# Kernel tuning notes

Measured on AMD Instinct MI355X. Metric: run time of the kernel, lower is better.

## Reference

```python
import jax, jax.numpy as jnp
import numpy as np

N = 50000      # nodes
E = 800000     # edges (before self loops)
F_IN = 128
HID = 32
HEADS = 4
C = 64         # num_classes
SLOPE = 0.2    # LeakyReLU negative slope (PyG GATConv default)


def setup_inputs() -> dict:
    key = jax.random.key(0)
    ks = jax.random.split(key, 16)
    def nrm(k, shape, scale=0.1):
        return jax.random.normal(k, shape, jnp.float32) * scale
    x = jax.random.normal(ks[0], (N, F_IN), jnp.float32)
    edge_index = jax.random.randint(ks[1], (2, E), 0, N, jnp.int32)
    # layer 1: F_IN -> HID per head, concat -> HEADS*HID
    w1 = nrm(ks[2], (F_IN, HEADS * HID)); as1 = nrm(ks[3], (HEADS, HID)); ad1 = nrm(ks[4], (HEADS, HID)); b1 = nrm(ks[5], (HEADS * HID,))
    # layer 2: HEADS*HID -> HID per head, concat
    w2 = nrm(ks[6], (HEADS * HID, HEADS * HID)); as2 = nrm(ks[7], (HEADS, HID)); ad2 = nrm(ks[8], (HEADS, HID)); b2 = nrm(ks[9], (HEADS * HID,))
    # layer 3: HEADS*HID -> C, single head, no concat (mean)
    w3 = nrm(ks[10], (HEADS * HID, C)); as3 = nrm(ks[11], (1, C)); ad3 = nrm(ks[12], (1, C)); b3 = nrm(ks[13], (C,))
    return {"x": x, "edge_index": edge_index,
            "w1": w1, "as1": as1, "ad1": ad1, "b1": b1,
            "w2": w2, "as2": as2, "ad2": ad2, "b2": b2,
            "w3": w3, "as3": as3, "ad3": ad3, "b3": b3}


def gat_conv(x, src, dst, W, a_src, a_dst, bias, heads, oc, concat):
    n = x.shape[0]
    h = (x @ W).reshape(n, heads, oc)                       # [N,H,F]
    al_s = jnp.einsum('nhf,hf->nh', h, a_src)               # [N,H]
    al_d = jnp.einsum('nhf,hf->nh', h, a_dst)
    e = jax.nn.leaky_relu(al_s[src] + al_d[dst], SLOPE)     # [E,H]
    # segment softmax over incoming edges per destination node
    m = jax.ops.segment_max(e, dst, num_segments=n)
    e = jnp.exp(e - m[dst])
    denom = jax.ops.segment_sum(e, dst, num_segments=n)
    alpha = e / denom[dst]                                  # [E,H]
    out = jax.ops.segment_sum(h[src] * alpha[:, :, None], dst, num_segments=n)  # [N,H,F]
    out = out.reshape(n, heads * oc) if concat else out.mean(axis=1)
    return out + bias


def reference(x, edge_index, w1, as1, ad1, b1, w2, as2, ad2, b2, w3, as3, ad3, b3):
    n = x.shape[0]
    loops = jnp.arange(n, dtype=edge_index.dtype)
    src = jnp.concatenate([edge_index[0], loops])           # add self loops (PyG default)
    dst = jnp.concatenate([edge_index[1], loops])
    h = gat_conv(x, src, dst, w1, as1, ad1, b1, HEADS, HID, True)
    h = jax.nn.relu(h)                                      # dropout is identity in eval
    h = gat_conv(h, src, dst, w2, as2, ad2, b2, HEADS, HID, True)
    h = jax.nn.relu(h)
    h = gat_conv(h, src, dst, w3, as3, ad3, b3, 1, C, False)
    return jax.nn.log_softmax(h, axis=1)
```

## Files before the change

### kernel.cpp

```cpp
#include <hip/hip_runtime.h>
#include <hip/hip_bf16.h>
#include <math.h>

#define SLOPE 0.2f
typedef unsigned int uint_t;
typedef unsigned short ushort_t;

static __device__ __forceinline__ float lrelu(float v) { return v > 0.f ? v : SLOPE * v; }
static __device__ __forceinline__ ushort_t f2b(float f) {
  uint_t u = __float_as_uint(f);
  u += 0x7fffu + ((u >> 16) & 1u);
  return (ushort_t)(u >> 16);
}


__global__ __launch_bounds__(256) void hist_kernel(const int* __restrict__ ei,
                                                   int* __restrict__ ts,
                                                   int E, int N, int NB, int NBUCK) {
  __shared__ int h[256];
  int tid = threadIdx.x, b = blockIdx.x;
  h[tid] = 0;
  __syncthreads();
  int ET = E + N;
  int base = b * 4096;
#pragma unroll
  for (int j = 0; j < 16; ++j) {
    int i = base + j * 256 + tid;
    if (i < ET) {
      int d = (i < E) ? ei[E + i] : (i - E);
      atomicAdd(&h[d >> 8], 1);
    }
  }
  __syncthreads();
  if (tid < NBUCK) ts[tid * NB + b] = h[tid];
}

__global__ __launch_bounds__(256) void scan1(int* __restrict__ a, int* __restrict__ bsum, int L) {
  int tid = threadIdx.x;
  int base = blockIdx.x * 1024 + tid * 4;
  int c0 = (base + 0 < L) ? a[base + 0] : 0;
  int c1 = (base + 1 < L) ? a[base + 1] : 0;
  int c2 = (base + 2 < L) ? a[base + 2] : 0;
  int c3 = (base + 3 < L) ? a[base + 3] : 0;
  int s = c0 + c1 + c2 + c3;
  int lane = tid & 63, wid = tid >> 6;
  int pre = s;
#pragma unroll
  for (int off = 1; off < 64; off <<= 1) {
    int t = __shfl_up(pre, off);
    if (lane >= off) pre += t;
  }
  __shared__ int wsum[4];
  if (lane == 63) wsum[wid] = pre;
  __syncthreads();
  int woff = 0;
#pragma unroll
  for (int w = 0; w < 4; ++w) woff += (w < wid) ? wsum[w] : 0;
  int excl = woff + pre - s;
  if (base + 0 < L) a[base + 0] = excl;
  if (base + 1 < L) a[base + 1] = excl + c0;
  if (base + 2 < L) a[base + 2] = excl + c0 + c1;
  if (base + 3 < L) a[base + 3] = excl + c0 + c1 + c2;
  if (tid == 255) bsum[blockIdx.x] = wsum[0] + wsum[1] + wsum[2] + wsum[3];
}

__global__ __launch_bounds__(1024) void scan2(int* __restrict__ bsum, int nb) {
  __shared__ int sh[1024];
  int tid = threadIdx.x;
  int v = (tid < nb) ? bsum[tid] : 0;
  sh[tid] = v;
  __syncthreads();
  for (int off = 1; off < 1024; off <<= 1) {
    int add = (tid >= off) ? sh[tid - off] : 0;
    __syncthreads();
    sh[tid] += add;
    __syncthreads();
  }
  if (tid < nb) bsum[tid] = sh[tid] - v;
}

__global__ __launch_bounds__(256) void scan3(int* __restrict__ a, const int* __restrict__ bsum, int L) {
  int tid = threadIdx.x;
  int base = blockIdx.x * 1024 + tid * 4;
  if (base >= L) return;
  int off = bsum[blockIdx.x];
#pragma unroll
  for (int j = 0; j < 4; ++j)
    if (base + j < L) a[base + j] += off;
}

__global__ __launch_bounds__(256) void part_kernel(const int* __restrict__ ei,
                                                   const int* __restrict__ ts,
                                                   uint_t* __restrict__ tmp,
                                                   int E, int N, int NB, int NBUCK) {
  __shared__ int bin[256];
  int tid = threadIdx.x, b = blockIdx.x;
  if (tid < NBUCK) bin[tid] = ts[tid * NB + b];
  __syncthreads();
  int ET = E + N;
  int base = b * 4096;
#pragma unroll
  for (int j = 0; j < 16; ++j) {
    int i = base + j * 256 + tid;
    if (i < ET) {
      int s, d;
      if (i < E) { s = ei[i]; d = ei[E + i]; } else { s = i - E; d = i - E; }
      int pos = atomicAdd(&bin[d >> 8], 1);
      tmp[pos] = ((uint_t)d << 16) | (uint_t)s;
    }
  }
}

__global__ __launch_bounds__(256) void bucket_kernel(const uint_t* __restrict__ tmp,
                                                     const int* __restrict__ ts,
                                                     int* __restrict__ rowptr,
                                                     int* __restrict__ esrc,
                                                     int N, int NB, int NBUCK, int ET) {
  __shared__ int h[256], pref[256], rank[256];
  __shared__ int wsum[4];
  int tid = threadIdx.x, d = blockIdx.x;
  int start = ts[d * NB];
  int end = (d == NBUCK - 1) ? ET : ts[(d + 1) * NB];
  h[tid] = 0; rank[tid] = 0;
  __syncthreads();
  for (int i = start + tid; i < end; i += 256)
    atomicAdd(&h[(tmp[i] >> 16) & 255], 1);
  __syncthreads();
  int v = h[tid];
  int lane = tid & 63, wid = tid >> 6;
  int inc = v;
#pragma unroll
  for (int off = 1; off < 64; off <<= 1) {
    int t = __shfl_up(inc, off);
    if (lane >= off) inc += t;
  }
  if (lane == 63) wsum[wid] = inc;
  __syncthreads();
  int woff = 0;
#pragma unroll
  for (int w = 0; w < 4; ++w) woff += (w < wid) ? wsum[w] : 0;
  pref[tid] = woff + inc - v;
  __syncthreads();
  int idx = d * 256 + tid;
  if (idx <= N) rowptr[idx] = start + pref[tid];
  for (int i = start + tid; i < end; i += 256) {
    uint_t v2 = tmp[i];
    int low = (v2 >> 16) & 255;
    int r = atomicAdd(&rank[low], 1);
    esrc[start + pref[low] + r] = (int)(v2 & 0xffffu);
  }
}


template<int OC, bool BF16IN>
__global__ __launch_bounds__(256) void gemm_tile(const void* __restrict__ Xv,
                                                 const float* __restrict__ W,
                                                 ushort_t* __restrict__ H, int N) {
  const int K = 128;
  const int CT = OC / 4;
  const int RPT = 64 / (256 / CT);
  __shared__ float xs[K][68];
  int tid = threadIdx.x;
  long row0 = (long)blockIdx.x * 64;
  if (BF16IN) {
    const ushort_t* X = (const ushort_t*)Xv;
#pragma unroll
    for (int i = 0; i < 4; ++i) {
      int flat = i * 256 + tid;
      int r = flat & 63, kc = flat >> 6;
      long row = row0 + r;
      long rr = row < N ? row : (long)(N - 1);
      uint4 v = *(const uint4*)(X + rr * K + kc * 8);
      uint_t vv[4] = {v.x, v.y, v.z, v.w};
#pragma unroll
      for (int j = 0; j < 4; ++j) {
        xs[kc * 8 + j * 2 + 0][r] = __uint_as_float(vv[j] << 16);
        xs[kc * 8 + j * 2 + 1][r] = __uint_as_float(vv[j] & 0xffff0000u);
      }
    }
  } else {
    const float* X = (const float*)Xv;
#pragma unroll
    for (int i = 0; i < 8; ++i) {
      int flat = i * 256 + tid;
      int r = flat & 63, kc = flat >> 6;
      long row = row0 + r;
      long rr = row < N ? row : (long)(N - 1);
      float4 xv = *(const float4*)(X + rr * K + kc * 4);
      xs[kc * 4 + 0][r] = xv.x;
      xs[kc * 4 + 1][r] = xv.y;
      xs[kc * 4 + 2][r] = xv.z;
      xs[kc * 4 + 3][r] = xv.w;
    }
  }
  __syncthreads();
  int ct = tid % CT;
  int rg = tid / CT;
  int c0 = ct * 4;
  int r0 = rg * RPT;
  float acc[RPT][4];
#pragma unroll
  for (int i = 0; i < RPT; ++i)
    for (int j = 0; j < 4; ++j) acc[i][j] = 0.f;
#pragma unroll 4
  for (int k = 0; k < K; ++k) {
    float4 wv = *(const float4*)(W + (long)k * OC + c0);
    const float4* xr = (const float4*)(&xs[k][r0]);
#pragma unroll
    for (int i4 = 0; i4 < RPT / 4; ++i4) {
      float4 xv = xr[i4];
      float xa[4] = {xv.x, xv.y, xv.z, xv.w};
#pragma unroll
      for (int j = 0; j < 4; ++j) {
        int i = i4 * 4 + j;
        acc[i][0] = fmaf(xa[j], wv.x, acc[i][0]);
        acc[i][1] = fmaf(xa[j], wv.y, acc[i][1]);
        acc[i][2] = fmaf(xa[j], wv.z, acc[i][2]);
        acc[i][3] = fmaf(xa[j], wv.w, acc[i][3]);
      }
    }
  }
#pragma unroll
  for (int i = 0; i < RPT; ++i) {
    long row = row0 + r0 + i;
    if (row < N) {
      ushort4 o = {f2b(acc[i][0]), f2b(acc[i][1]), f2b(acc[i][2]), f2b(acc[i][3])};
      *(ushort4*)(H + row * OC + c0) = o;
    }
  }
}


__global__ void al_kernel4(const ushort_t* __restrict__ h, const float* __restrict__ a_s,
                           const float* __restrict__ a_d, float* __restrict__ als,
                           float* __restrict__ ald, int N) {
  int tid = threadIdx.x;
  int n = blockIdx.x * 16 + (tid >> 4);
  int sl = tid & 15, hd = sl >> 2;
  if (n >= N) return;
  uint4 v = *(const uint4*)(h + (long)n * 128 + sl * 8);
  uint_t vv[4] = {v.x, v.y, v.z, v.w};
  const float* sp = a_s + hd * 32 + (sl & 3) * 8;
  const float* dp = a_d + hd * 32 + (sl & 3) * 8;
  float vs = 0.f, vd = 0.f;
#pragma unroll
  for (int j = 0; j < 4; ++j) {
    float h0 = __uint_as_float(vv[j] << 16);
    float h1 = __uint_as_float(vv[j] & 0xffff0000u);
    vs = fmaf(h0, sp[j * 2 + 0], vs); vs = fmaf(h1, sp[j * 2 + 1], vs);
    vd = fmaf(h0, dp[j * 2 + 0], vd); vd = fmaf(h1, dp[j * 2 + 1], vd);
  }
#pragma unroll
  for (int off = 1; off <= 2; off <<= 1) {
    vs += __shfl_xor(vs, off);
    vd += __shfl_xor(vd, off);
  }
  if ((sl & 3) == 0) { als[(long)n * 4 + hd] = vs; ald[(long)n * 4 + hd] = vd; }
}

__global__ void al_kernel1(const ushort_t* __restrict__ h, const float* __restrict__ a_s,
                           const float* __restrict__ a_d, float* __restrict__ als,
                           float* __restrict__ ald, int N) {
  int tid = threadIdx.x;
  int n = blockIdx.x * 32 + (tid >> 3);
  int sl = tid & 7;
  if (n >= N) return;
  uint4 v = *(const uint4*)(h + (long)n * 64 + sl * 8);
  uint_t vv[4] = {v.x, v.y, v.z, v.w};
  const float* sp = a_s + sl * 8;
  const float* dp = a_d + sl * 8;
  float vs = 0.f, vd = 0.f;
#pragma unroll
  for (int j = 0; j < 4; ++j) {
    float h0 = __uint_as_float(vv[j] << 16);
    float h1 = __uint_as_float(vv[j] & 0xffff0000u);
    vs = fmaf(h0, sp[j * 2 + 0], vs); vs = fmaf(h1, sp[j * 2 + 1], vs);
    vd = fmaf(h0, dp[j * 2 + 0], vd); vd = fmaf(h1, dp[j * 2 + 1], vd);
  }
#pragma unroll
  for (int off = 1; off <= 4; off <<= 1) {
    vs += __shfl_xor(vs, off);
    vd += __shfl_xor(vd, off);
  }
  if (sl == 0) { als[n] = vs; ald[n] = vd; }
}


__global__ __launch_bounds__(256) void gat_agg128(const ushort_t* __restrict__ h,
    const float* __restrict__ als, const float* __restrict__ ald,
    const int* __restrict__ rowptr, const int* __restrict__ esrc,
    const float* __restrict__ bias, ushort_t* __restrict__ out, int N) {
  int tid = threadIdx.x;
  int n = blockIdx.x * 8 + (tid >> 5);
  int l = tid & 31;
  int slot = l >> 4, sl = l & 15, hd = sl >> 2;
  if (n >= N) return;
  int beg = rowptr[n], end = rowptr[n + 1];
  float aldv = ald[(long)n * 4 + hd];
  float den = 0.f;
  float acc[8] = {0.f, 0.f, 0.f, 0.f, 0.f, 0.f, 0.f, 0.f};
  for (int e = beg + slot; e < end; e += 2) {
    int s = esrc[e];
    float p = __expf(lrelu(als[(long)s * 4 + hd] + aldv));
    den += p;
    uint4 v = *(const uint4*)(h + (long)s * 128 + sl * 8);
    uint_t vv[4] = {v.x, v.y, v.z, v.w};
#pragma unroll
    for (int j = 0; j < 4; ++j) {
      acc[2 * j + 0] = fmaf(p, __uint_as_float(vv[j] << 16), acc[2 * j + 0]);
      acc[2 * j + 1] = fmaf(p, __uint_as_float(vv[j] & 0xffff0000u), acc[2 * j + 1]);
    }
  }
  den += __shfl_xor(den, 16);
#pragma unroll
  for (int j = 0; j < 8; ++j) acc[j] += __shfl_xor(acc[j], 16);
  if (slot == 0) {
    float inv = 1.f / den;
    float4 bv0 = *(const float4*)(bias + sl * 8);
    float4 bv1 = *(const float4*)(bias + sl * 8 + 4);
    float bb[8] = {bv0.x, bv0.y, bv0.z, bv0.w, bv1.x, bv1.y, bv1.z, bv1.w};
    uint_t pk[4];
#pragma unroll
    for (int j = 0; j < 4; ++j) {
      float v0 = fmaxf(fmaf(acc[2 * j + 0], inv, bb[2 * j + 0]), 0.f);
      float v1 = fmaxf(fmaf(acc[2 * j + 1], inv, bb[2 * j + 1]), 0.f);
      pk[j] = (uint_t)f2b(v0) | ((uint_t)f2b(v1) << 16);
    }
    uint4 pv = {pk[0], pk[1], pk[2], pk[3]};
    *(uint4*)(out + (long)n * 128 + sl * 8) = pv;
  }
}

__global__ __launch_bounds__(256) void gat_agg64_lsm(const ushort_t* __restrict__ h,
    const float* __restrict__ als, const float* __restrict__ ald,
    const int* __restrict__ rowptr, const int* __restrict__ esrc,
    const float* __restrict__ bias, float* __restrict__ out, int N) {
  int tid = threadIdx.x;
  int n = blockIdx.x * 8 + (tid >> 5);
  int l = tid & 31;
  int slot = l >> 3, sl = l & 7;
  if (n >= N) return;
  int beg = rowptr[n], end = rowptr[n + 1];
  float aldv = ald[n];
  float den = 0.f;
  float acc[8] = {0.f, 0.f, 0.f, 0.f, 0.f, 0.f, 0.f, 0.f};
  for (int e = beg + slot; e < end; e += 4) {
    int s = esrc[e];
    float p = __expf(lrelu(als[s] + aldv));
    den += p;
    uint4 v = *(const uint4*)(h + (long)s * 64 + sl * 8);
    uint_t vv[4] = {v.x, v.y, v.z, v.w};
#pragma unroll
    for (int j = 0; j < 4; ++j) {
      acc[2 * j + 0] = fmaf(p, __uint_as_float(vv[j] << 16), acc[2 * j + 0]);
      acc[2 * j + 1] = fmaf(p, __uint_as_float(vv[j] & 0xffff0000u), acc[2 * j + 1]);
    }
  }
  den += __shfl_xor(den, 8); den += __shfl_xor(den, 16);
#pragma unroll
  for (int j = 0; j < 8; ++j) {
    acc[j] += __shfl_xor(acc[j], 8);
    acc[j] += __shfl_xor(acc[j], 16);
  }
  if (slot == 0) {
    float inv = 1.f / den;
    float v[8];
#pragma unroll
    for (int j = 0; j < 8; ++j) v[j] = fmaf(acc[j], inv, bias[sl * 8 + j]);
    float lm = v[0];
#pragma unroll
    for (int j = 1; j < 8; ++j) lm = fmaxf(lm, v[j]);
#pragma unroll
    for (int off = 1; off <= 4; off <<= 1) lm = fmaxf(lm, __shfl_xor(lm, off));
    float es = 0.f;
#pragma unroll
    for (int j = 0; j < 8; ++j) es += __expf(v[j] - lm);
#pragma unroll
    for (int off = 1; off <= 4; off <<= 1) es += __shfl_xor(es, off);
    float lse = lm + __logf(es);
    float4 o0 = {v[0] - lse, v[1] - lse, v[2] - lse, v[3] - lse};
    float4 o1 = {v[4] - lse, v[5] - lse, v[6] - lse, v[7] - lse};
    *(float4*)(out + (long)n * 64 + sl * 8 + 0) = o0;
    *(float4*)(out + (long)n * 64 + sl * 8 + 4) = o1;
  }
}


extern "C" void kernel_launch(void* const* d_in, const int* in_sizes, int n_in,
                              void* d_out, int out_size, void* d_ws, size_t ws_size,
                              hipStream_t stream) {
  const float* x   = (const float*)d_in[0];
  const int*   ei  = (const int*)d_in[1];
  const float* w1  = (const float*)d_in[2];
  const float* as1 = (const float*)d_in[3];
  const float* ad1 = (const float*)d_in[4];
  const float* b1  = (const float*)d_in[5];
  const float* w2  = (const float*)d_in[6];
  const float* as2 = (const float*)d_in[7];
  const float* ad2 = (const float*)d_in[8];
  const float* b2  = (const float*)d_in[9];
  const float* w3  = (const float*)d_in[10];
  const float* as3 = (const float*)d_in[11];
  const float* ad3 = (const float*)d_in[12];
  const float* b3  = (const float*)d_in[13];
  float* out = (float*)d_out;

  const int N = in_sizes[0] / 128;
  const int E = in_sizes[1] / 2;
  const int ET = E + N;

  const int NB = (ET + 4095) / 4096;
  const int NBUCK = (N + 255) >> 8;
  const int SL = NBUCK * NB;
  const int nsb = (SL + 1023) / 1024;

  char* ws = (char*)d_ws;
  size_t off = 0;
  auto alloc = [&](size_t bytes) -> void* {
    void* p = ws + off;
    off += (bytes + 255) & ~(size_t)255;
    return p;
  };
  ushort_t* bufA = (ushort_t*)alloc((size_t)N * 128 * 2);
  ushort_t* bufB = (ushort_t*)alloc((size_t)N * 128 * 2);
  float* als   = (float*)alloc((size_t)N * 4 * 4);
  float* ald   = (float*)alloc((size_t)N * 4 * 4);
  int* ts      = (int*)alloc((size_t)SL * 4);
  int* bsum    = (int*)alloc((size_t)1024 * 4);
  uint_t* tmp  = (uint_t*)alloc((size_t)ET * 4);
  int* rowptr  = (int*)alloc((size_t)(N + 1) * 4);
  int* esrc    = (int*)alloc((size_t)ET * 4);

  const int ggrid = (N + 63) / 64;
  const int albk = (N + 15) / 16;
  const int aggrid = (N + 7) / 8;

  hist_kernel<<<NB, 256, 0, stream>>>(ei, ts, E, N, NB, NBUCK);
  scan1<<<nsb, 256, 0, stream>>>(ts, bsum, SL);
  scan2<<<1, 1024, 0, stream>>>(bsum, nsb);
  scan3<<<nsb, 256, 0, stream>>>(ts, bsum, SL);
  part_kernel<<<NB, 256, 0, stream>>>(ei, ts, tmp, E, N, NB, NBUCK);
  bucket_kernel<<<NBUCK, 256, 0, stream>>>(tmp, ts, rowptr, esrc, N, NB, NBUCK, ET);

  gemm_tile<128, false><<<ggrid, 256, 0, stream>>>(x, w1, bufA, N);
  al_kernel4<<<albk, 256, 0, stream>>>(bufA, as1, ad1, als, ald, N);
  gat_agg128<<<aggrid, 256, 0, stream>>>(bufA, als, ald, rowptr, esrc, b1, bufB, N);

  gemm_tile<128, true><<<ggrid, 256, 0, stream>>>(bufB, w2, bufA, N);
  al_kernel4<<<albk, 256, 0, stream>>>(bufA, as2, ad2, als, ald, N);
  gat_agg128<<<aggrid, 256, 0, stream>>>(bufA, als, ald, rowptr, esrc, b2, bufB, N);

  gemm_tile<64, true><<<ggrid, 256, 0, stream>>>(bufB, w3, bufA, N);
  al_kernel1<<<(N + 31) / 32, 256, 0, stream>>>(bufA, as3, ad3, als, ald, N);
  gat_agg64_lsm<<<aggrid, 256, 0, stream>>>(bufA, als, ald, rowptr, esrc, b3, out, N);
}
```

Before: 325.0 us.

## Merge independent graph-build kernels with layer-1 GEMM and attention logits

Combines the edge histogram with the first-layer GEMM in one launch, and combines the scan fix-up with the layer-1 attention-logit kernel, splitting blocks by index range. This cuts two kernel launches and lets independent work share the GPU, which helps fill otherwise underused small launches. It also swaps manual bf16 bit-shift unpacking for the __bfloat1622float2 intrinsic. The fused GEMM/hist kernel keeps the larger GEMM shared-memory footprint for every block, which may reduce occupancy for the histogram blocks.

Measured after the change: 315.7 us. -2.9%, faster.

```diff
diff --git a/kernel.cpp b/kernel.cpp
--- a/kernel.cpp
+++ b/kernel.cpp
@@ -12,13 +12,17 @@
   u += 0x7fffu + ((u >> 16) & 1u);
   return (ushort_t)(u >> 16);
 }
-
-
-__global__ __launch_bounds__(256) void hist_kernel(const int* __restrict__ ei,
-                                                   int* __restrict__ ts,
-                                                   int E, int N, int NB, int NBUCK) {
+static __device__ __forceinline__ float2 b2x2(uint_t u) {
+  union { uint_t u; __hip_bfloat162 b; } cv;
+  cv.u = u;
+  return __bfloat1622float2(cv.b);
+}
+
+
+__device__ __forceinline__ void hist_body(const int* __restrict__ ei, int* __restrict__ ts,
+                                          int E, int N, int NB, int NBUCK, int b) {
   __shared__ int h[256];
-  int tid = threadIdx.x, b = blockIdx.x;
+  int tid = threadIdx.x;
   h[tid] = 0;
   __syncthreads();
   int ET = E + N;
@@ -79,11 +83,12 @@
   if (tid < nb) bsum[tid] = sh[tid] - v;
 }
 
-__global__ __launch_bounds__(256) void scan3(int* __restrict__ a, const int* __restrict__ bsum, int L) {
-  int tid = threadIdx.x;
-  int base = blockIdx.x * 1024 + tid * 4;
+__device__ __forceinline__ void scan3_body(int* __restrict__ a, const int* __restrict__ bsum,
+                                           int L, int b) {
+  int tid = threadIdx.x;
+  int base = b * 1024 + tid * 4;
   if (base >= L) return;
-  int off = bsum[blockIdx.x];
+  int off = bsum[b];
 #pragma unroll
   for (int j = 0; j < 4; ++j)
     if (base + j < L) a[base + j] += off;
@@ -153,15 +158,15 @@
 
 
 template<int OC, bool BF16IN>
-__global__ __launch_bounds__(256) void gemm_tile(const void* __restrict__ Xv,
-                                                 const float* __restrict__ W,
-                                                 ushort_t* __restrict__ H, int N) {
+__device__ __forceinline__ void gemm_body(const void* __restrict__ Xv,
+                                          const float* __restrict__ W,
+                                          ushort_t* __restrict__ H, int N, int bid) {
   const int K = 128;
   const int CT = OC / 4;
   const int RPT = 64 / (256 / CT);
   __shared__ float xs[K][68];
   int tid = threadIdx.x;
-  long row0 = (long)blockIdx.x * 64;
+  long row0 = (long)bid * 64;
   if (BF16IN) {
     const ushort_t* X = (const ushort_t*)Xv;
 #pragma unroll
@@ -174,8 +179,9 @@
       uint_t vv[4] = {v.x, v.y, v.z, v.w};
 #pragma unroll
       for (int j = 0; j < 4; ++j) {
-        xs[kc * 8 + j * 2 + 0][r] = __uint_as_float(vv[j] << 16);
-        xs[kc * 8 + j * 2 + 1][r] = __uint_as_float(vv[j] & 0xffff0000u);
+        float2 f = b2x2(vv[j]);
+        xs[kc * 8 + j * 2 + 0][r] = f.x;
+        xs[kc * 8 + j * 2 + 1][r] = f.y;
       }
     }
   } else {
@@ -230,12 +236,30 @@
   }
 }
 
-
-__global__ void al_kernel4(const ushort_t* __restrict__ h, const float* __restrict__ a_s,
-                           const float* __restrict__ a_d, float* __restrict__ als,
-                           float* __restrict__ ald, int N) {
-  int tid = threadIdx.x;
-  int n = blockIdx.x * 16 + (tid >> 4);
+template<int OC, bool BF16IN>
+__global__ __launch_bounds__(256) void gemm_tile(const void* __restrict__ Xv,
+                                                 const float* __restrict__ W,
+                                                 ushort_t* __restrict__ H, int N) {
+  gemm_body<OC, BF16IN>(Xv, W, H, N, blockIdx.x);
+}
+
+__global__ __launch_bounds__(256) void k_gemm1_hist(const float* __restrict__ X,
+    const float* __restrict__ W, ushort_t* __restrict__ H, int N,
+    const int* __restrict__ ei, int* __restrict__ ts, int E, int NB, int NBUCK,
+    int gemmBlocks) {
+  int bid = blockIdx.x;
+  if (bid < gemmBlocks) gemm_body<128, false>(X, W, H, N, bid);
+  else hist_body(ei, ts, E, N, NB, NBUCK, bid - gemmBlocks);
+}
+
+
+__device__ __forceinline__ void al4_body(const ushort_t* __restrict__ h,
+                                         const float* __restrict__ a_s,
+                                         const float* __restrict__ a_d,
+                                         float* __restrict__ als, float* __restrict__ ald,
+                                         int N, int bid) {
+  int tid = threadIdx.x;
+  int n = bid * 16 + (tid >> 4);
   int sl = tid & 15, hd = sl >> 2;
   if (n >= N) return;
   uint4 v = *(const uint4*)(h + (long)n * 128 + sl * 8);
@@ -245,10 +269,9 @@
   float vs = 0.f, vd = 0.f;
 #pragma unroll
   for (int j = 0; j < 4; ++j) {
-    float h0 = __uint_as_float(vv[j] << 16);
-    float h1 = __uint_as_float(vv[j] & 0xffff0000u);
-    vs = fmaf(h0, sp[j * 2 + 0], vs); vs = fmaf(h1, sp[j * 2 + 1], vs);
-    vd = fmaf(h0, dp[j * 2 + 0], vd); vd = fmaf(h1, dp[j * 2 + 1], vd);
+    float2 f = b2x2(vv[j]);
+    vs = fmaf(f.x, sp[j * 2 + 0], vs); vs = fmaf(f.y, sp[j * 2 + 1], vs);
+    vd = fmaf(f.x, dp[j * 2 + 0], vd); vd = fmaf(f.y, dp[j * 2 + 1], vd);
   }
 #pragma unroll
   for (int off = 1; off <= 2; off <<= 1) {
@@ -256,6 +279,21 @@
     vd += __shfl_xor(vd, off);
   }
   if ((sl & 3) == 0) { als[(long)n * 4 + hd] = vs; ald[(long)n * 4 + hd] = vd; }
+}
+
+__global__ void al_kernel4(const ushort_t* __restrict__ h, const float* __restrict__ a_s,
+                           const float* __restrict__ a_d, float* __restrict__ als,
+                           float* __restrict__ ald, int N) {
+  al4_body(h, a_s, a_d, als, ald, N, blockIdx.x);
+}
+
+__global__ __launch_bounds__(256) void k_scan3_al4(int* __restrict__ a,
+    const int* __restrict__ bsum, int L, int scanBlocks,
+    const ushort_t* __restrict__ h, const float* __restrict__ a_s,
+    const float* __restrict__ a_d, float* __restrict__ als, float* __restrict__ ald, int N) {
+  int bid = blockIdx.x;
+  if (bid < scanBlocks) scan3_body(a, bsum, L, bid);
+  else al4_body(h, a_s, a_d, als, ald, N, bid - scanBlocks);
 }
 
 __global__ void al_kernel1(const ushort_t* __restrict__ h, const float* __restrict__ a_s,
@@ -272,10 +310,9 @@
   float vs = 0.f, vd = 0.f;
 #pragma unroll
   for (int j = 0; j < 4; ++j) {
-    float h0 = __uint_as_float(vv[j] << 16);
-    float h1 = __uint_as_float(vv[j] & 0xffff0000u);
-    vs = fmaf(h0, sp[j * 2 + 0], vs); vs = fmaf(h1, sp[j * 2 + 1], vs);
-    vd = fmaf(h0, dp[j * 2 + 0], vd); vd = fmaf(h1, dp[j * 2 + 1], vd);
+    float2 f = b2x2(vv[j]);
+    vs = fmaf(f.x, sp[j * 2 + 0], vs); vs = fmaf(f.y, sp[j * 2 + 1], vs);
+    vd = fmaf(f.x, dp[j * 2 + 0], vd); vd = fmaf(f.y, dp[j * 2 + 1], vd);
   }
 #pragma unroll
   for (int off = 1; off <= 4; off <<= 1) {
@@ -307,8 +344,9 @@
     uint_t vv[4] = {v.x, v.y, v.z, v.w};
 #pragma unroll
     for (int j = 0; j < 4; ++j) {
-      acc[2 * j + 0] = fmaf(p, __uint_as_float(vv[j] << 16), acc[2 * j + 0]);
-      acc[2 * j + 1] = fmaf(p, __uint_as_float(vv[j] & 0xffff0000u), acc[2 * j + 1]);
+      float2 f = b2x2(vv[j]);
+      acc[2 * j + 0] = fmaf(p, f.x, acc[2 * j + 0]);
+      acc[2 * j + 1] = fmaf(p, f.y, acc[2 * j + 1]);
     }
   }
   den += __shfl_xor(den, 16);
@@ -352,8 +390,9 @@
     uint_t vv[4] = {v.x, v.y, v.z, v.w};
 #pragma unroll
     for (int j = 0; j < 4; ++j) {
-      acc[2 * j + 0] = fmaf(p, __uint_as_float(vv[j] << 16), acc[2 * j + 0]);
-      acc[2 * j + 1] = fmaf(p, __uint_as_float(vv[j] & 0xffff0000u), acc[2 * j + 1]);
+      float2 f = b2x2(vv[j]);
+      acc[2 * j + 0] = fmaf(p, f.x, acc[2 * j + 0]);
+      acc[2 * j + 1] = fmaf(p, f.y, acc[2 * j + 1]);
     }
   }
   den += __shfl_xor(den, 8); den += __shfl_xor(den, 16);
@@ -435,15 +474,14 @@
   const int albk = (N + 15) / 16;
   const int aggrid = (N + 7) / 8;
 
-  hist_kernel<<<NB, 256, 0, stream>>>(ei, ts, E, N, NB, NBUCK);
+  k_gemm1_hist<<<ggrid + NB, 256, 0, stream>>>(x, w1, bufA, N, ei, ts, E, NB, NBUCK, ggrid);
   scan1<<<nsb, 256, 0, stream>>>(ts, bsum, SL);
   scan2<<<1, 1024, 0, stream>>>(bsum, nsb);
-  scan3<<<nsb, 256, 0, stream>>>(ts, bsum, SL);
+  k_scan3_al4<<<nsb + albk, 256, 0, stream>>>(ts, bsum, SL, nsb,
+                                              bufA, as1, ad1, als, ald, N);
   part_kernel<<<NB, 256, 0, stream>>>(ei, ts, tmp, E, N, NB, NBUCK);
   bucket_kernel<<<NBUCK, 256, 0, stream>>>(tmp, ts, rowptr, esrc, N, NB, NBUCK, ET);
 
-  gemm_tile<128, false><<<ggrid, 256, 0, stream>>>(x, w1, bufA, N);
-  al_kernel4<<<albk, 256, 0, stream>>>(bufA, as1, ad1, als, ald, N);
   gat_agg128<<<aggrid, 256, 0, stream>>>(bufA, als, ald, rowptr, esrc, b1, bufB, N);
 
   gemm_tile<128, true><<<ggrid, 256, 0, stream>>>(bufB, w2, bufA, N);
```
